# Performance work log

Measured on AMD Instinct MI355X. Metric: run time of the kernel, lower is better.

## Reference

```python
import jax, jax.numpy as jnp
import numpy as np
import math

H = 65
W = 65
NH = 8
DIM_K = 512
DIM_Q = 512
DIM_HID = NH * DIM_K  # 4096; forced by V.view(bsz,-1,num_heads,dim_K)
RW = W // 2 + 1  # 33, rfft2 last-dim size


def _conv2d(x, w, pad):
    # x: NCHW, w: OIHW
    return jax.lax.conv_general_dilated(
        x, w, window_strides=(1, 1), padding=[(pad, pad), (pad, pad)],
        dimension_numbers=('NCHW', 'OIHW', 'NCHW'))


def _filter_branch(x, w1, w2, w3, Wd, bd):
    # x: (1, DIM_K, H, W)
    f = _conv2d(x, w1, 0)                                  # 1x1 conv
    f = _conv2d(jax.nn.relu(f), w2, 1) + f                 # 3x3 conv + residual
    f = jax.nn.relu(_conv2d(jax.nn.relu(f), w3, 0))        # 1x1 -> (1, NH, H, W)
    f = f.reshape(NH, H * W) @ Wd.T + bd                   # down-proj to (NH, 65*33)
    return f.reshape(NH, H, RW)


def setup_inputs() -> dict:
    key = jax.random.key(0)
    ks = jax.random.split(key, 20)
    s = 0.02
    f32 = jnp.float32
    inp = {
        'Q': jax.random.normal(ks[0], (1, 1, DIM_Q), f32),
        'K': jax.random.normal(ks[1], (1, DIM_K, H, W), f32),
        'Wq': jax.random.normal(ks[2], (DIM_HID, DIM_Q), f32) * s,
        'bq': jnp.zeros((DIM_HID,), f32),
        'Wk': jax.random.normal(ks[3], (DIM_HID, DIM_K), f32) * s,
        'bk': jnp.zeros((DIM_HID,), f32),
        'Wv': jax.random.normal(ks[4], (DIM_HID, DIM_K), f32) * s,
        'bv': jnp.zeros((DIM_HID,), f32),
        'Wo': jax.random.normal(ks[5], (DIM_K, DIM_HID), f32) * s,
        'bo': jnp.zeros((DIM_K,), f32),
        'amp1': jax.random.normal(ks[6], (DIM_K, DIM_K, 1, 1), f32) * 0.05,
        'amp2': jax.random.normal(ks[7], (DIM_K, DIM_K, 3, 3), f32) * 0.02,
        'amp3': jax.random.normal(ks[8], (NH, DIM_K, 1, 1), f32) * 0.05,
        'pha1': jax.random.normal(ks[9], (DIM_K, DIM_K, 1, 1), f32) * 0.05,
        'pha2': jax.random.normal(ks[10], (DIM_K, DIM_K, 3, 3), f32) * 0.02,
        'pha3': jax.random.normal(ks[11], (NH, DIM_K, 1, 1), f32) * 0.05,
        'Wd1': jax.random.normal(ks[12], (H * RW, H * W), f32) * s,
        'bd1': jnp.zeros((H * RW,), f32),
        'Wd2': jax.random.normal(ks[13], (H * RW, H * W), f32) * s,
        'bd2': jnp.zeros((H * RW,), f32),
    }
    return inp


def reference(Q, K, Wq, bq, Wk, bk, Wv, bv, Wo, bo,
              amp1, amp2, amp3, pha1, pha2, pha3, Wd1, bd1, Wd2, bd2):
    bsz, h, w = K.shape[0], K.shape[2], K.shape[3]
    dk = DIM_HID // NH
    qrt = K
    Kp = jnp.transpose(K, (0, 2, 3, 1))                      # (1, h, w, DIM_K)
    q = Q @ Wq.T + bq                                        # (1, 1, DIM_HID)
    k = Kp @ Wk.T + bk                                       # (1, h, w, DIM_HID)
    v = Kp @ Wv.T + bv
    q = q.reshape(bsz, -1, NH, dk).transpose(0, 2, 1, 3)     # (1, NH, 1, dk)
    k = k.reshape(bsz, -1, NH, dk).transpose(0, 2, 1, 3)     # (1, NH, h*w, dk)
    v = v.reshape(bsz, -1, NH, DIM_K).transpose(0, 2, 1, 3)  # (1, NH, h*w, DIM_K)
    A = jnp.einsum('bhqd,bhkd->bhqk', q, k) / math.sqrt(DIM_K)
    amp_F = _filter_branch(qrt, amp1, amp2, amp3, Wd1, bd1)  # (NH, h, w//2+1)
    pha_F = _filter_branch(qrt, pha1, pha2, pha3, Wd2, bd2)
    A = A.reshape(NH, h, w)
    Af = jnp.fft.rfft2(A, axes=(-2, -1))                     # backward norm (default)
    amp = amp_F * jnp.abs(Af)
    pha = pha_F * jnp.angle(Af)
    Af = jax.lax.complex(amp * jnp.cos(pha), amp * jnp.sin(pha))
    A = jnp.fft.irfft2(Af, s=(h, w), axes=(-2, -1))
    A = jax.nn.softmax(A.reshape(bsz, NH, 1, -1), axis=-1)   # (1, NH, 1, h*w)
    x = jnp.einsum('bhqk,bhkd->bhqd', A, v)                  # (1, NH, 1, DIM_K)
    x = x.reshape(1, NH * DIM_K)
    return x @ Wo.T + bo                                     # (1, DIM_K)
```

## Files before the change

kernel.cpp:

```cpp
#include <hip/hip_runtime.h>
#include <hip/hip_bf16.h>

#define NP 4225
#define PR 2145

typedef __attribute__((ext_vector_type(8))) short short8;
typedef __attribute__((ext_vector_type(4))) float f32x4;
typedef __attribute__((ext_vector_type(4))) unsigned int u32x4;

__device__ inline float bf2f(unsigned short u) {
    union { unsigned int i; float f; } x; x.i = ((unsigned int)u) << 16; return x.f;
}
__device__ inline unsigned short f2bf(float f) {
    union { float f; unsigned int i; } x; x.f = f;
    unsigned int r = x.i + 0x7fff + ((x.i >> 16) & 1);
    return (unsigned short)(r >> 16);
}
__device__ inline u32x4 relu8(u32x4 v) {
    #pragma unroll
    for (int i = 0; i < 4; i++) {
        unsigned int s = v[i] & 0x80008000u;
        v[i] &= ~((s >> 15) * 0xFFFFu);
    }
    return v;
}
__device__ inline void gl_lds16(const void* g, void* l) {
    __builtin_amdgcn_global_load_lds(
        (const __attribute__((address_space(1))) unsigned int*)g,
        (__attribute__((address_space(3))) unsigned int*)l,
        16, 0, 0);
}


__global__ __launch_bounds__(256) void k_q(const float* __restrict__ Q,
                                           const float* __restrict__ Wq,
                                           const float* __restrict__ bq,
                                           float* __restrict__ qv)
{
    int wid = threadIdx.x >> 6, lane = threadIdx.x & 63;
    int j = blockIdx.x * 4 + wid;
    float s = 0.f;
    for (int i = lane; i < 512; i += 64) s += Q[i] * Wq[j * 512 + i];
    #pragma unroll
    for (int off = 32; off; off >>= 1) s += __shfl_down(s, off);
    if (lane == 0) qv[j] = s + bq[j];
}

__global__ __launch_bounds__(256) void k_qk3(const float* __restrict__ qv,
                                             const float* __restrict__ Wk,
                                             float* __restrict__ qkp)
{
    int c = blockIdx.x * 256 + threadIdx.x;
    int h = blockIdx.y, dz = blockIdx.z;
    __shared__ float qs[32];
    if (threadIdx.x < 32) qs[threadIdx.x] = qv[h * 512 + dz * 32 + threadIdx.x];
    __syncthreads();
    float s = 0.f;
    #pragma unroll 8
    for (int d = 0; d < 32; d++)
        s += qs[d] * Wk[(size_t)(h * 512 + dz * 32 + d) * 512 + c];
    qkp[(dz * 8 + h) * 512 + c] = s;
}

__global__ __launch_bounds__(512) void k_qb(const float* __restrict__ q,
                                            const float* __restrict__ bk,
                                            float* __restrict__ qb)
{
    int h = threadIdx.x >> 6, lane = threadIdx.x & 63;
    float s = 0.f;
    for (int d = lane; d < 512; d += 64) s += q[h * 512 + d] * bk[h * 512 + d];
    #pragma unroll
    for (int off = 32; off; off >>= 1) s += __shfl_down(s, off);
    if (lane == 0) qb[h] = s;
}

__global__ __launch_bounds__(256) void k_alogits3(const float* __restrict__ qkp,
                                                  const float* __restrict__ K,
                                                  float* __restrict__ Ap)
{
    __shared__ float sqk[8][16];
    int tid = threadIdx.x;
    int cz = blockIdx.y;
    if (tid < 128) {
        int hh = tid >> 4, cc = tid & 15;
        float s = 0.f;
        #pragma unroll
        for (int dz = 0; dz < 16; dz++) s += qkp[(dz * 8 + hh) * 512 + cz * 16 + cc];
        sqk[hh][cc] = s;
    }
    __syncthreads();
    int p = blockIdx.x * 256 + tid;
    bool ok = p < NP;
    float acc[8] = {};
    #pragma unroll
    for (int cc = 0; cc < 16; cc++) {
        float kv = ok ? K[(size_t)(cz * 16 + cc) * NP + p] : 0.f;
        #pragma unroll
        for (int h = 0; h < 8; h++) acc[h] += sqk[h][cc] * kv;
    }
    if (ok) {
        #pragma unroll
        for (int h = 0; h < 8; h++) Ap[(size_t)(cz * 8 + h) * NP + p] = acc[h];
    }
}

__global__ __launch_bounds__(256) void k_areduce(const float* __restrict__ Ap,
                                                 const float* __restrict__ qb,
                                                 float* __restrict__ A)
{
    int p = blockIdx.x * 256 + threadIdx.x;
    int h = blockIdx.y;
    if (p >= NP) return;
    float s = 0.f;
    #pragma unroll 8
    for (int cz = 0; cz < 32; cz++) s += Ap[(size_t)(cz * 8 + h) * NP + p];
    const float sc = 0.04419417382415922f;
    A[h * NP + p] = (s + qb[h]) * sc;
}


__global__ __launch_bounds__(256) void k_cast2(const float* __restrict__ a,
                                               const float* __restrict__ b,
                                               unsigned short* __restrict__ o)
{
    int i = blockIdx.x * 256 + threadIdx.x;
    int br = blockIdx.y;
    const float* src = br ? b : a;
    int m = i >> 9, c = i & 511;
    int dst = (c & ~63) | ((c & 63) ^ ((m & 7) << 3));
    o[(size_t)br * 262144 + m * 512 + dst] = f2bf(src[i]);
}

__global__ __launch_bounds__(256) void k_packW2(const float* __restrict__ a,
                                                const float* __restrict__ b,
                                                unsigned short* __restrict__ o)
{
    int i = blockIdx.x * 256 + threadIdx.x;
    int br = blockIdx.y;
    int m = i >> 9, c = i & 511;
    const float* src = (br ? b : a) + (size_t)i * 9;
    unsigned short* dst = o + (size_t)br * 512 * 4608;
    int cs = (c & ~63) | ((c & 63) ^ ((m & 7) << 3));
    #pragma unroll
    for (int t = 0; t < 9; t++) dst[(size_t)m * 4608 + t * 512 + cs] = f2bf(src[t]);
}


__global__ __launch_bounds__(256) void k_conv1T(const float* __restrict__ K,
                                                const unsigned short* __restrict__ w1b2,
                                                unsigned short* __restrict__ f0b2)
{
    __shared__ unsigned short As[2][64 * 64];
    __shared__ unsigned short Bs[2][128 * 64];
    int tid = threadIdx.x;
    int bid = blockIdx.x;
    int u = bid & 7;
    int t = bid >> 3;
    int bmi = u * 9 + t % 9;
    if (bmi >= 67) return;
    int combo = t / 9;
    int bm = bmi * 64;
    int bn = (combo & 3) * 128;
    int br = combo >> 2;
    const unsigned short* w1 = w1b2 + (size_t)br * 262144;
    unsigned short* f0 = f0b2 + (size_t)br * NP * 512;
    int lane = tid & 63;
    int w = tid >> 6;
    int wp = (w >> 1) * 32, wm = (w & 1) * 64;
    int ct = tid >> 4, p4 = (tid & 15) * 4;

    bool okj[4];
    int colj[4];
    #pragma unroll
    for (int j = 0; j < 4; j++) {
        okj[j] = (bm + p4 + j) < NP;
        colj[j] = okj[j] ? (p4 + j) : (NP - 1 - bm);
    }

    f32x4 acc[2][4];
    #pragma unroll
    for (int i = 0; i < 2; i++)
        #pragma unroll
        for (int j = 0; j < 4; j++) acc[i][j] = (f32x4){0.f, 0.f, 0.f, 0.f};

    float aE[16], aO[16];

    auto loadA = [&](int kc, float (&ar)[16]) {
        int c0 = kc * 64;
        #pragma unroll
        for (int pass = 0; pass < 4; pass++) {
            int cl = pass * 16 + ct;
            const float* src = K + (size_t)(c0 + cl) * NP + bm;
            #pragma unroll
            for (int j = 0; j < 4; j++) ar[pass * 4 + j] = src[colj[j]];
        }
    };
    auto writeA = [&](int buf, float (&ar)[16]) {
        #pragma unroll
        for (int pass = 0; pass < 4; pass++) {
            int cl = pass * 16 + ct;
            #pragma unroll
            for (int j = 0; j < 4; j++) {
                int row = p4 + j;
                int byte = (row * 128 + cl * 2) ^ ((row & 7) << 4);
                float v = okj[j] ? ar[pass * 4 + j] : 0.f;
                *(unsigned short*)((char*)As[buf] + byte) = f2bf(v);
            }
        }
    };
    auto stageB = [&](int kc, int buf) {
        const unsigned short* gb = w1 + (size_t)kc * 64 + (lane & 7) * 8;
        #pragma unroll
        for (int j = 0; j < 4; j++) {
            int row = (w * 4 + j) * 8 + (lane >> 3);
            gl_lds16(gb + (size_t)(bn + row) * 512,
                     (char*)Bs[buf] + (w * 4 + j) * 1024);
        }
    };
    auto mfmaStep = [&](int buf) {
        __builtin_amdgcn_s_setprio(1);
        #pragma unroll
        for (int ks = 0; ks < 2; ks++) {
            short8 af[2], bfr[4];
            #pragma unroll
            for (int fi = 0; fi < 2; fi++) {
                int row = wp + fi * 16 + (lane & 15);
                int byte = row * 128 + ((ks * 64 + ((lane >> 4) * 16)) ^ ((row & 7) << 4));
                af[fi] = *(const short8*)((char*)As[buf] + byte);
            }
            #pragma unroll
            for (int fj = 0; fj < 4; fj++) {
                int n = wm + fj * 16 + (lane & 15);
                int byte = n * 128 + ((ks * 64 + ((lane >> 4) * 16)) ^ ((n & 7) << 4));
                bfr[fj] = *(const short8*)((char*)Bs[buf] + byte);
            }
            #pragma unroll
            for (int fi = 0; fi < 2; fi++)
                #pragma unroll
                for (int fj = 0; fj < 4; fj++)
                    acc[fi][fj] = __builtin_amdgcn_mfma_f32_16x16x32_bf16(af[fi], bfr[fj], acc[fi][fj], 0, 0, 0);
        }
        __builtin_amdgcn_s_setprio(0);
    };

    loadA(0, aE);
    loadA(1, aO);
    stageB(0, 0);
    writeA(0, aE);
    __syncthreads();
    #pragma unroll
    for (int ib = 0; ib < 4; ib++) {
        int s0 = 2 * ib;
        if (s0 + 1 < 8) stageB(s0 + 1, 1);
        if (s0 + 2 < 8) loadA(s0 + 2, aE);
        mfmaStep(0);
        if (s0 + 1 < 8) writeA(1, aO);
        __syncthreads();
        int s1 = s0 + 1;
        if (s1 + 1 < 8) stageB(s1 + 1, 0);
        if (s1 + 2 < 8) loadA(s1 + 2, aO);
        mfmaStep(1);
        if (s1 + 1 < 8) writeA(0, aE);
        __syncthreads();
    }
    #pragma unroll
    for (int fi = 0; fi < 2; fi++)
        #pragma unroll
        for (int r = 0; r < 4; r++) {
            int p = bm + wp + fi * 16 + (lane >> 4) * 4 + r;
            if (p >= NP) continue;
            #pragma unroll
            for (int fj = 0; fj < 4; fj++) {
                int m = bn + wm + fj * 16 + (lane & 15);
                f0[(size_t)p * 512 + m] = f2bf(acc[fi][fj][r]);
            }
        }
}

__global__ __launch_bounds__(256) void k_conv3T(const unsigned short* __restrict__ f0b2,
                                                const unsigned short* __restrict__ w2b2,
                                                const float* __restrict__ amp3,
                                                const float* __restrict__ pha3,
                                                float* __restrict__ F2p)
{
    __shared__ unsigned short As[2][64 * 64];
    __shared__ unsigned short Bs[2][128 * 64];
    __shared__ float w3s[8 * 128];
    int tid = threadIdx.x;
    int bid = blockIdx.x;
    int u = bid & 7;
    int bmi = bid >> 3;
    if (bmi >= 67) return;
    int bm = bmi * 64;
    int bnq = u & 3;
    int bn = bnq * 128;
    int br = u >> 2;
    const unsigned short* f0 = f0b2 + (size_t)br * NP * 512;
    const unsigned short* w2 = w2b2 + (size_t)br * 512 * 4608;
    const float* w3 = br ? pha3 : amp3;
    for (int i = tid; i < 1024; i += 256) {
        int h = i >> 7, c = i & 127;
        w3s[i] = w3[h * 512 + bn + c];
    }
    int lane = tid & 63;
    int w = tid >> 6;
    int wp = (w >> 1) * 32, wm = (w & 1) * 64;
    int ra = tid >> 2, sa = tid & 3;
    int pA = bm + ra;
    int py = pA / 65, px = pA - py * 65;

    f32x4 acc[2][4];
    #pragma unroll
    for (int i = 0; i < 2; i++)
        #pragma unroll
        for (int j = 0; j < 4; j++) acc[i][j] = (f32x4){0.f, 0.f, 0.f, 0.f};

    u32x4 aE0, aE1, aO0, aO1;
    bool vE, vO;

    auto loadA = [&](int s, u32x4& a0, u32x4& a1, bool& vv) {
        int kc = s / 9, tap = s - kc * 9;
        int ky = tap / 3 - 1, kx = tap % 3 - 1;
        int sy = py + ky, sx = px + kx;
        bool valid = (pA < NP) && sy >= 0 && sy < 65 && sx >= 0 && sx < 65;
        int srow = valid ? (pA + ky * 65 + kx) : 0;
        const unsigned short* arow = f0 + (size_t)srow * 512 + kc * 64 + sa * 16;
        a0 = *(const u32x4*)arow;
        a1 = *(const u32x4*)(arow + 8);
        vv = valid;
    };
    auto writeA = [&](int buf, u32x4 a0, u32x4 a1, bool vv) {
        u32x4 z = {0, 0, 0, 0};
        u32x4 w0 = vv ? relu8(a0) : z;
        u32x4 w1 = vv ? relu8(a1) : z;
        int ab = ra * 128 + sa * 32;
        int swz = (ra & 7) << 4;
        *(u32x4*)((char*)As[buf] + (ab ^ swz)) = w0;
        *(u32x4*)((char*)As[buf] + ((ab + 16) ^ swz)) = w1;
    };
    auto stageB = [&](int s, int buf) {
        int kc = s / 9, tap = s - kc * 9;
        const unsigned short* gb = w2 + (size_t)tap * 512 + kc * 64 + (lane & 7) * 8;
        #pragma unroll
        for (int j = 0; j < 4; j++) {
            int row = (w * 4 + j) * 8 + (lane >> 3);
            gl_lds16(gb + (size_t)(bn + row) * 4608,
                     (char*)Bs[buf] + (w * 4 + j) * 1024);
        }
    };
    auto mfmaStep = [&](int buf) {
        __builtin_amdgcn_s_setprio(1);
        #pragma unroll
        for (int ks = 0; ks < 2; ks++) {
            short8 af[2], bfr[4];
            #pragma unroll
            for (int fi = 0; fi < 2; fi++) {
                int row = wp + fi * 16 + (lane & 15);
                int byte = row * 128 + ((ks * 64 + ((lane >> 4) * 16)) ^ ((row & 7) << 4));
                af[fi] = *(const short8*)((char*)As[buf] + byte);
            }
            #pragma unroll
            for (int fj = 0; fj < 4; fj++) {
                int n = wm + fj * 16 + (lane & 15);
                int byte = n * 128 + ((ks * 64 + ((lane >> 4) * 16)) ^ ((n & 7) << 4));
                bfr[fj] = *(const short8*)((char*)Bs[buf] + byte);
            }
            #pragma unroll
            for (int fi = 0; fi < 2; fi++)
                #pragma unroll
                for (int fj = 0; fj < 4; fj++)
                    acc[fi][fj] = __builtin_amdgcn_mfma_f32_16x16x32_bf16(af[fi], bfr[fj], acc[fi][fj], 0, 0, 0);
        }
        __builtin_amdgcn_s_setprio(0);
    };

    loadA(0, aE0, aE1, vE);
    loadA(1, aO0, aO1, vO);
    stageB(0, 0);
    writeA(0, aE0, aE1, vE);
    __syncthreads();
    for (int ib = 0; ib < 36; ib++) {
        int s0 = 2 * ib;
        if (s0 + 1 < 72) stageB(s0 + 1, 1);
        if (s0 + 2 < 72) loadA(s0 + 2, aE0, aE1, vE);
        mfmaStep(0);
        if (s0 + 1 < 72) writeA(1, aO0, aO1, vO);
        __syncthreads();
        int s1 = s0 + 1;
        if (s1 + 1 < 72) stageB(s1 + 1, 0);
        if (s1 + 2 < 72) loadA(s1 + 2, aO0, aO1, vO);
        mfmaStep(1);
        if (s1 + 1 < 72) writeA(0, aE0, aE1, vE);
        __syncthreads();
    }
    #pragma unroll
    for (int fi = 0; fi < 2; fi++)
        #pragma unroll
        for (int r = 0; r < 4; r++) {
            int row = wp + fi * 16 + (lane >> 4) * 4 + r;
            int p = bm + row;
            #pragma unroll
            for (int fj = 0; fj < 4; fj++) {
                int mcol = wm + fj * 16 + (lane & 15);
                float v = 0.f;
                if (p < NP)
                    v = fmaxf(acc[fi][fj][r] + bf2f(f0[(size_t)p * 512 + bn + mcol]), 0.f);
                int byte = (row * 256 + mcol * 2) ^ ((row & 7) << 4);
                *(unsigned short*)((char*)Bs[0] + byte) = f2bf(v);
            }
        }
    __syncthreads();
    int pl = tid >> 2, qc = tid & 3;
    float a8[8] = {};
    #pragma unroll 4
    for (int jj = 0; jj < 16; jj++) {
        int c = qc * 32 + jj * 2;
        int byte = (pl * 256 + c * 2) ^ ((pl & 7) << 4);
        unsigned int uu = *(const unsigned int*)((char*)Bs[0] + byte);
        float v0 = bf2f((unsigned short)(uu & 0xFFFF));
        float v1 = bf2f((unsigned short)(uu >> 16));
        #pragma unroll
        for (int h = 0; h < 8; h++)
            a8[h] += w3s[h * 128 + c] * v0 + w3s[h * 128 + c + 1] * v1;
    }
    #pragma unroll
    for (int h = 0; h < 8; h++) {
        a8[h] += __shfl_xor(a8[h], 1);
        a8[h] += __shfl_xor(a8[h], 2);
    }
    int p = bm + pl;
    if (qc == 0 && p < NP) {
        float* dst = F2p + (size_t)(br * 4 + bnq) * 8 * NP;
        #pragma unroll
        for (int h = 0; h < 8; h++) dst[h * NP + p] = a8[h];
    }
}

__global__ __launch_bounds__(256) void k_f2red(const float* __restrict__ F2p,
                                               float* __restrict__ F2)
{
    int p = blockIdx.x * 256 + threadIdx.x;
    int h = blockIdx.y, br = blockIdx.z;
    if (p >= NP) return;
    float s = 0.f;
    #pragma unroll
    for (int bn = 0; bn < 4; bn++) s += F2p[(size_t)((br * 4 + bn) * 8 + h) * NP + p];
    F2[(size_t)(br * 8 + h) * NP + p] = fmaxf(s, 0.f);
}

__global__ __launch_bounds__(256) void k_down(const float* __restrict__ F2,
                                              const float* __restrict__ Wd1,
                                              const float* __restrict__ bd1,
                                              const float* __restrict__ Wd2,
                                              const float* __restrict__ bd2,
                                              float* __restrict__ Fa,
                                              float* __restrict__ Fp)
{
    int wid = threadIdx.x >> 6, lane = threadIdx.x & 63;
    int j = blockIdx.x * 4 + wid;
    if (j >= PR) return;
    int br = blockIdx.y;
    const float* Wd = br ? Wd2 : Wd1;
    const float* bd = br ? bd2 : bd1;
    const float* F2b = F2 + (size_t)br * 8 * NP;
    float* Fo = br ? Fp : Fa;
    const float* wr = Wd + (size_t)j * NP;
    float acc[8] = {};
    for (int p = lane; p < NP; p += 64) {
        float wv = wr[p];
        #pragma unroll
        for (int h = 0; h < 8; h++) acc[h] += wv * F2b[h * NP + p];
    }
    #pragma unroll
    for (int h = 0; h < 8; h++) {
        #pragma unroll
        for (int off = 32; off; off >>= 1) acc[h] += __shfl_down(acc[h], off);
    }
    if (lane == 0) {
        float b = bd[j];
        #pragma unroll
        for (int h = 0; h < 8; h++) Fo[h * PR + j] = acc[h] + b;
    }
}


__global__ __launch_bounds__(128) void k_twid(double* __restrict__ ctd, double* __restrict__ snd,
                                              float* __restrict__ ctf, float* __restrict__ stf)
{
    int t = threadIdx.x;
    if (t < 65) {
        double ang = 6.283185307179586476925286766559 * (double)t / 65.0;
        double cv = cos(ang), sv = sin(ang);
        ctd[t] = cv; snd[t] = sv;
        ctf[t] = (float)cv; stf[t] = (float)sv;
    }
}

__global__ __launch_bounds__(64) void k_fftA(const float* __restrict__ A,
                                             const double* __restrict__ ctd,
                                             const double* __restrict__ snd,
                                             float* __restrict__ TrG, float* __restrict__ TiG)
{
    int b = blockIdx.x;
    int h = b / 65, y = b % 65;
    int lane = threadIdx.x;
    __shared__ float rowA[65];
    __shared__ double c65[65], s65[65];
    rowA[lane] = A[h * NP + y * 65 + lane];
    c65[lane] = ctd[lane]; s65[lane] = snd[lane];
    if (lane == 0) {
        rowA[64] = A[h * NP + y * 65 + 64];
        c65[64] = ctd[64]; s65[64] = snd[64];
    }
    __syncthreads();
    int v = lane;
    if (v < 33) {
        double sr = 0.0, si = 0.0;
        for (int x = 0; x < 65; x++) {
            int m = (v * x) % 65;
            double a = (double)rowA[x];
            sr += a * c65[m];
            si -= a * s65[m];
        }
        TrG[(h * 65 + y) * 33 + v] = (float)sr;
        TiG[(h * 65 + y) * 33 + v] = (float)si;
    }
}

__global__ __launch_bounds__(128) void k_fftBC(const float* __restrict__ TrG,
                                               const float* __restrict__ TiG,
                                               const float* __restrict__ Fa,
                                               const float* __restrict__ Fp,
                                               const double* __restrict__ ctd,
                                               const double* __restrict__ snd,
                                               const float* __restrict__ ctf,
                                               const float* __restrict__ stf,
                                               float* __restrict__ CrG, float* __restrict__ CiG)
{
    int v = blockIdx.x, h = blockIdx.y;
    int t = threadIdx.x;
    __shared__ float TrS[65], TiS[65];
    __shared__ float BrS[65], BiS[65];
    __shared__ double c65[65], s65[65];
    __shared__ float cf[65], sf[65];
    if (t < 65) {
        TrS[t] = TrG[(h * 65 + t) * 33 + v];
        TiS[t] = TiG[(h * 65 + t) * 33 + v];
        c65[t] = ctd[t]; s65[t] = snd[t];
        cf[t] = ctf[t]; sf[t] = stf[t];
    }
    __syncthreads();
    int uu = t;
    if (uu < 65) {
        double sr = 0.0, si = 0.0;
        for (int y = 0; y < 65; y++) {
            int m = (uu * y) % 65;
            double c = c65[m], s = s65[m];
            double tr = (double)TrS[y], ti = (double)TiS[y];
            sr += tr * c + ti * s;
            si += ti * c - tr * s;
        }
        float re = (float)sr, im = (float)si;
        float mag = sqrtf(re * re + im * im);
        float ang = atan2f(im, re);
        int o = uu * 33 + v;
        float amp = Fa[h * PR + o] * mag;
        float ph  = Fp[h * PR + o] * ang;
        float sn, cn;
        sincosf(ph, &sn, &cn);
        BrS[uu] = amp * cn;
        BiS[uu] = amp * sn;
    }
    __syncthreads();
    int y = t;
    if (y < 65) {
        float sr = 0.f, si = 0.f;
        for (int u2 = 0; u2 < 65; u2++) {
            int m = (u2 * y) % 65;
            float c = cf[m], s = sf[m];
            float ar = BrS[u2], ai = BiS[u2];
            sr += ar * c - ai * s;
            si += ai * c + ar * s;
        }
        CrG[(h * 65 + y) * 33 + v] = sr;
        CiG[(h * 65 + y) * 33 + v] = si;
    }
}

__global__ __launch_bounds__(128) void k_fftD(const float* __restrict__ CrG,
                                              const float* __restrict__ CiG,
                                              const float* __restrict__ ctf,
                                              const float* __restrict__ stf,
                                              float* __restrict__ A2)
{
    int y = blockIdx.x, h = blockIdx.y;
    int t = threadIdx.x;
    __shared__ float CrS[33], CiS[33];
    __shared__ float c65[65], s65[65];
    if (t < 33) {
        CrS[t] = CrG[(h * 65 + y) * 33 + t];
        CiS[t] = CiG[(h * 65 + y) * 33 + t];
    }
    if (t < 65) { c65[t] = ctf[t]; s65[t] = stf[t]; }
    __syncthreads();
    int x = t;
    if (x < 65) {
        float s = CrS[0];
        for (int v = 1; v < 33; v++) {
            int m = (v * x) % 65;
            s += 2.f * (CrS[v] * c65[m] - CiS[v] * s65[m]);
        }
        A2[h * NP + y * 65 + x] = s * (1.f / 4225.f);
    }
}

__global__ __launch_bounds__(1024) void k_softmax(const float* __restrict__ A2,
                                                  float* __restrict__ Wsm)
{
    int h = blockIdx.x, tid = threadIdx.x;
    __shared__ float red[1024];
    float mx = -3.0e38f;
    for (int i = tid; i < NP; i += 1024) mx = fmaxf(mx, A2[h * NP + i]);
    red[tid] = mx; __syncthreads();
    for (int s = 512; s; s >>= 1) {
        if (tid < s) red[tid] = fmaxf(red[tid], red[tid + s]);
        __syncthreads();
    }
    mx = red[0]; __syncthreads();
    float sum = 0.f;
    for (int i = tid; i < NP; i += 1024) sum += expf(A2[h * NP + i] - mx);
    red[tid] = sum; __syncthreads();
    for (int s = 512; s; s >>= 1) {
        if (tid < s) red[tid] += red[tid + s];
        __syncthreads();
    }
    float inv = 1.f / red[0];
    for (int i = tid; i < NP; i += 1024) Wsm[h * NP + i] = expf(A2[h * NP + i] - mx) * inv;
}

__global__ __launch_bounds__(256) void k_t(const float* __restrict__ K,
                                           const float* __restrict__ Wsm,
                                           float* __restrict__ t)
{
    int wid = threadIdx.x >> 6, lane = threadIdx.x & 63;
    int c = blockIdx.x * 4 + wid;
    float acc[8] = {};
    for (int p = lane; p < NP; p += 64) {
        float kv = K[(size_t)c * NP + p];
        #pragma unroll
        for (int h = 0; h < 8; h++) acc[h] += kv * Wsm[h * NP + p];
    }
    #pragma unroll
    for (int h = 0; h < 8; h++) {
        #pragma unroll
        for (int off = 32; off; off >>= 1) acc[h] += __shfl_down(acc[h], off);
    }
    if (lane == 0) {
        #pragma unroll
        for (int h = 0; h < 8; h++) t[h * 512 + c] = acc[h];
    }
}

__global__ __launch_bounds__(256) void k_x(const float* __restrict__ t,
                                           const float* __restrict__ Wv,
                                           const float* __restrict__ bv,
                                           float* __restrict__ x)
{
    int wid = threadIdx.x >> 6, lane = threadIdx.x & 63;
    int hd = blockIdx.x * 4 + wid;
    int h = hd >> 9;
    float s = 0.f;
    for (int c = lane; c < 512; c += 64) s += t[h * 512 + c] * Wv[(size_t)hd * 512 + c];
    #pragma unroll
    for (int off = 32; off; off >>= 1) s += __shfl_down(s, off);
    if (lane == 0) x[hd] = s + bv[hd];
}

__global__ __launch_bounds__(256) void k_out(const float* __restrict__ x,
                                             const float* __restrict__ Wo,
                                             const float* __restrict__ bo,
                                             float* __restrict__ out)
{
    int wid = threadIdx.x >> 6, lane = threadIdx.x & 63;
    int j = blockIdx.x * 4 + wid;
    float s = 0.f;
    for (int i = lane; i < 4096; i += 64) s += x[i] * Wo[(size_t)j * 4096 + i];
    #pragma unroll
    for (int off = 32; off; off >>= 1) s += __shfl_down(s, off);
    if (lane == 0) out[j] = s + bo[j];
}

extern "C" void kernel_launch(void* const* d_in, const int* in_sizes, int n_in,
                              void* d_out, int out_size, void* d_ws, size_t ws_size,
                              hipStream_t stream)
{
    (void)in_sizes; (void)n_in; (void)out_size; (void)ws_size;
    const float* Q    = (const float*)d_in[0];
    const float* K    = (const float*)d_in[1];
    const float* Wq   = (const float*)d_in[2];
    const float* bq   = (const float*)d_in[3];
    const float* Wk   = (const float*)d_in[4];
    const float* bk   = (const float*)d_in[5];
    const float* Wv   = (const float*)d_in[6];
    const float* bv   = (const float*)d_in[7];
    const float* Wo   = (const float*)d_in[8];
    const float* bo   = (const float*)d_in[9];
    const float* amp1 = (const float*)d_in[10];
    const float* amp2 = (const float*)d_in[11];
    const float* amp3 = (const float*)d_in[12];
    const float* pha1 = (const float*)d_in[13];
    const float* pha2 = (const float*)d_in[14];
    const float* pha3 = (const float*)d_in[15];
    const float* Wd1  = (const float*)d_in[16];
    const float* bd1  = (const float*)d_in[17];
    const float* Wd2  = (const float*)d_in[18];
    const float* bd2  = (const float*)d_in[19];
    float* out = (float*)d_out;

    char* w = (char*)d_ws;
    auto alloc = [&](size_t bytes) { char* p = w; w += (bytes + 255) & ~(size_t)255; return p; };
    float* qv   = (float*)alloc(4096 * 4);
    float* qkp  = (float*)alloc(16 * 8 * 512 * 4);
    float* qb   = (float*)alloc(64 * 4);
    float* A    = (float*)alloc(8 * NP * 4);
    unsigned short* w1b2 = (unsigned short*)alloc((size_t)2 * 512 * 512 * 2);
    unsigned short* w2b2 = (unsigned short*)alloc((size_t)2 * 512 * 4608 * 2);
    unsigned short* f0b2 = (unsigned short*)alloc((size_t)2 * NP * 512 * 2);
    float* F2p  = (float*)alloc((size_t)2 * 4 * 8 * NP * 4);
    float* F2   = (float*)alloc((size_t)2 * 8 * NP * 4);
    float* Fa   = (float*)alloc(8 * PR * 4);
    float* Fp   = (float*)alloc(8 * PR * 4);
    double* ctd = (double*)alloc(65 * 8);
    double* snd = (double*)alloc(65 * 8);
    float* ctf  = (float*)alloc(65 * 4);
    float* stf  = (float*)alloc(65 * 4);
    float* Ap   = (float*)w2b2;
    {
        char* s2 = (char*)f0b2;
        auto alias = [&](size_t bytes) { char* p = s2; s2 += (bytes + 255) & ~(size_t)255; return p; };
        float* A2  = (float*)alias(8 * NP * 4);
        float* wsm = (float*)alias(8 * NP * 4);
        float* tt  = (float*)alias(4096 * 4);
        float* xx  = (float*)alias(4096 * 4);
        float* TrG = (float*)alias(8 * PR * 4);
        float* TiG = (float*)alias(8 * PR * 4);
        float* CrG = (float*)alias(8 * PR * 4);
        float* CiG = (float*)alias(8 * PR * 4);

        k_twid<<<1, 128, 0, stream>>>(ctd, snd, ctf, stf);

        k_q<<<1024, 256, 0, stream>>>(Q, Wq, bq, qv);
        k_qk3<<<dim3(2, 8, 16), 256, 0, stream>>>(qv, Wk, qkp);
        k_qb<<<1, 512, 0, stream>>>(qv, bk, qb);
        k_alogits3<<<dim3(17, 32), 256, 0, stream>>>(qkp, K, Ap);
        k_areduce<<<dim3(17, 8), 256, 0, stream>>>(Ap, qb, A);

        k_cast2<<<dim3(1024, 2), 256, 0, stream>>>(amp1, pha1, w1b2);
        k_packW2<<<dim3(1024, 2), 256, 0, stream>>>(amp2, pha2, w2b2);

        k_conv1T<<<576, 256, 0, stream>>>(K, w1b2, f0b2);
        k_conv3T<<<536, 256, 0, stream>>>(f0b2, w2b2, amp3, pha3, F2p);
        k_f2red<<<dim3(17, 8, 2), 256, 0, stream>>>(F2p, F2);
        k_down<<<dim3(537, 2), 256, 0, stream>>>(F2, Wd1, bd1, Wd2, bd2, Fa, Fp);

        k_fftA<<<520, 64, 0, stream>>>(A, ctd, snd, TrG, TiG);
        k_fftBC<<<dim3(33, 8), 128, 0, stream>>>(TrG, TiG, Fa, Fp, ctd, snd, ctf, stf, CrG, CiG);
        k_fftD<<<dim3(65, 8), 128, 0, stream>>>(CrG, CiG, ctf, stf, A2);
        k_softmax<<<8, 1024, 0, stream>>>(A2, wsm);
        k_t<<<128, 256, 0, stream>>>(K, wsm, tt);
        k_x<<<1024, 256, 0, stream>>>(tt, Wv, bv, xx);
        k_out<<<128, 256, 0, stream>>>(xx, Wo, bo, out);
    }
}
```

Measured before the change: 252.4 us.

## Stage conv3x3 A tiles via direct global-to-LDS loads with pre-swizzled f0

The 3x3 conv kernel now loads its shifted activation rows straight into LDS with gl_lds16 instead of going through registers. The producer kernel writes f0 with a per-row XOR swizzle so that these raw copies land in a bank-conflict-free layout. Boundary masking and ReLU move into the MFMA fragment read, keyed on the tap shift. The aim is to cut register pressure and VALU work in the staging path. In exchange, every fragment read now repeats ReLU and validity checks, and the swizzle must match exactly across both kernels and the residual read.

Result: slower. 258.7 us (+2.5%).

```diff
diff --git a/kernel.cpp b/kernel.cpp
--- a/kernel.cpp
+++ b/kernel.cpp
@@ -272,7 +272,8 @@
             #pragma unroll
             for (int fj = 0; fj < 4; fj++) {
                 int m = bn + wm + fj * 16 + (lane & 15);
-                f0[(size_t)p * 512 + m] = f2bf(acc[fi][fj][r]);
+                int ms = (m & ~63) | ((m & 63) ^ ((p & 7) << 3));
+                f0[(size_t)p * 512 + ms] = f2bf(acc[fi][fj][r]);
             }
         }
 }
@@ -305,9 +306,8 @@
     int lane = tid & 63;
     int w = tid >> 6;
     int wp = (w >> 1) * 32, wm = (w & 1) * 64;
-    int ra = tid >> 2, sa = tid & 3;
-    int pA = bm + ra;
-    int py = pA / 65, px = pA - py * 65;
+    int pxf0 = (bm + wp + (lane & 15)) % 65;
+    int pxf1 = (bm + wp + 16 + (lane & 15)) % 65;
 
     f32x4 acc[2][4];
     #pragma unroll
@@ -315,28 +315,17 @@
         #pragma unroll
         for (int j = 0; j < 4; j++) acc[i][j] = (f32x4){0.f, 0.f, 0.f, 0.f};
 
-    u32x4 aE0, aE1, aO0, aO1;
-    bool vE, vO;
-
-    auto loadA = [&](int s, u32x4& a0, u32x4& a1, bool& vv) {
+    auto stageA = [&](int s, int buf) {
         int kc = s / 9, tap = s - kc * 9;
-        int ky = tap / 3 - 1, kx = tap % 3 - 1;
-        int sy = py + ky, sx = px + kx;
-        bool valid = (pA < NP) && sy >= 0 && sy < 65 && sx >= 0 && sx < 65;
-        int srow = valid ? (pA + ky * 65 + kx) : 0;
-        const unsigned short* arow = f0 + (size_t)srow * 512 + kc * 64 + sa * 16;
-        a0 = *(const u32x4*)arow;
-        a1 = *(const u32x4*)(arow + 8);
-        vv = valid;
-    };
-    auto writeA = [&](int buf, u32x4 a0, u32x4 a1, bool vv) {
-        u32x4 z = {0, 0, 0, 0};
-        u32x4 w0 = vv ? relu8(a0) : z;
-        u32x4 w1 = vv ? relu8(a1) : z;
-        int ab = ra * 128 + sa * 32;
-        int swz = (ra & 7) << 4;
-        *(u32x4*)((char*)As[buf] + (ab ^ swz)) = w0;
-        *(u32x4*)((char*)As[buf] + ((ab + 16) ^ swz)) = w1;
+        int shift = (tap / 3 - 1) * 65 + (tap % 3) - 1;
+        #pragma unroll
+        for (int j = 0; j < 2; j++) {
+            int r = j * 32 + w * 8 + (lane >> 3);
+            int g = bm + shift + r;
+            g = g < 0 ? 0 : (g >= NP ? NP - 1 : g);
+            gl_lds16(f0 + (size_t)g * 512 + kc * 64 + (lane & 7) * 8,
+                     (char*)As[buf] + j * 4096 + w * 1024);
+        }
     };
     auto stageB = [&](int s, int buf) {
         int kc = s / 9, tap = s - kc * 9;
@@ -348,7 +337,10 @@
                      (char*)Bs[buf] + (w * 4 + j) * 1024);
         }
     };
-    auto mfmaStep = [&](int buf) {
+    auto mfmaStep = [&](int buf, int s) {
+        int tap = s % 9;
+        int ky = tap / 3 - 1, kx = tap % 3 - 1;
+        int shift = ky * 65 + kx;
         __builtin_amdgcn_s_setprio(1);
         #pragma unroll
         for (int ks = 0; ks < 2; ks++) {
@@ -356,8 +348,18 @@
             #pragma unroll
             for (int fi = 0; fi < 2; fi++) {
                 int row = wp + fi * 16 + (lane & 15);
-                int byte = row * 128 + ((ks * 64 + ((lane >> 4) * 16)) ^ ((row & 7) << 4));
-                af[fi] = *(const short8*)((char*)As[buf] + byte);
+                int key = ((row + shift) & 7) << 4;
+                int byte = row * 128 + ((ks * 64 + ((lane >> 4) * 16)) ^ key);
+                u32x4 a = *(const u32x4*)((char*)As[buf] + byte);
+                int pin = bm + row + shift;
+                int px = fi ? pxf1 : pxf0;
+                bool ok = ((unsigned)pin < NP) &&
+                          !((kx < 0 && px == 0) || (kx > 0 && px == 64));
+                a = relu8(a);
+                u32x4 z = {0, 0, 0, 0};
+                a = ok ? a : z;
+                union { u32x4 u; short8 s8; } cv; cv.u = a;
+                af[fi] = cv.s8;
             }
             #pragma unroll
             for (int fj = 0; fj < 4; fj++) {
@@ -374,23 +376,15 @@
         __builtin_amdgcn_s_setprio(0);
     };
 
-    loadA(0, aE0, aE1, vE);
-    loadA(1, aO0, aO1, vO);
     stageB(0, 0);
-    writeA(0, aE0, aE1, vE);
-    __syncthreads();
-    for (int ib = 0; ib < 36; ib++) {
-        int s0 = 2 * ib;
-        if (s0 + 1 < 72) stageB(s0 + 1, 1);
-        if (s0 + 2 < 72) loadA(s0 + 2, aE0, aE1, vE);
-        mfmaStep(0);
-        if (s0 + 1 < 72) writeA(1, aO0, aO1, vO);
+    stageA(0, 0);
+    __syncthreads();
+    for (int s0 = 0; s0 < 72; s0 += 2) {
+        if (s0 + 1 < 72) { stageB(s0 + 1, 1); stageA(s0 + 1, 1); }
+        mfmaStep(0, s0);
         __syncthreads();
-        int s1 = s0 + 1;
-        if (s1 + 1 < 72) stageB(s1 + 1, 0);
-        if (s1 + 2 < 72) loadA(s1 + 2, aO0, aO1, vO);
-        mfmaStep(1);
-        if (s1 + 1 < 72) writeA(0, aE0, aE1, vE);
+        if (s0 + 2 < 72) { stageB(s0 + 2, 0); stageA(s0 + 2, 0); }
+        mfmaStep(1, s0 + 1);
         __syncthreads();
     }
     #pragma unroll
@@ -403,8 +397,11 @@
             for (int fj = 0; fj < 4; fj++) {
                 int mcol = wm + fj * 16 + (lane & 15);
                 float v = 0.f;
-                if (p < NP)
-                    v = fmaxf(acc[fi][fj][r] + bf2f(f0[(size_t)p * 512 + bn + mcol]), 0.f);
+                if (p < NP) {
+                    int m = bn + mcol;
+                    int ms = (m & ~63) | ((m & 63) ^ ((p & 7) << 3));
+                    v = fmaxf(acc[fi][fj][r] + bf2f(f0[(size_t)p * 512 + ms]), 0.f);
+                }
                 int byte = (row * 256 + mcol * 2) ^ ((row & 7) << 4);
                 *(unsigned short*)((char*)Bs[0] + byte) = f2bf(v);
             }
```

## Fuse small launches: merge q/qk/twiddle, areduce+fftA, atomic conv3 reduction

Applied to the files above, without the earlier changes.

Several small kernels are merged to cut launch count. The q projection, the q·Wk product and the twiddle table are folded into one kernel, and qb is recomputed per block inside the new reduce+row-DFT kernel. That kernel combines the A partial-sum reduction with the first FFT stage. The conv3T partial sums are now accumulated with atomicAdd into a memset-zeroed F2, and the ReLU moves into k_down, which removes the k_f2red pass. In exchange the q row dot products are recomputed redundantly across blocks, atomics add contention, and float summation order becomes nondeterministic.

Result: no change. 257.3 us (+1.9%).

```diff
diff --git a/kernel.cpp b/kernel.cpp
--- a/kernel.cpp
+++ b/kernel.cpp
@@ -32,46 +32,40 @@
 }
 
 
-__global__ __launch_bounds__(256) void k_q(const float* __restrict__ Q,
-                                           const float* __restrict__ Wq,
-                                           const float* __restrict__ bq,
-                                           float* __restrict__ qv)
-{
-    int wid = threadIdx.x >> 6, lane = threadIdx.x & 63;
-    int j = blockIdx.x * 4 + wid;
+__global__ __launch_bounds__(256) void k_qk4(const float* __restrict__ Q,
+                                             const float* __restrict__ Wq,
+                                             const float* __restrict__ bq,
+                                             const float* __restrict__ Wk,
+                                             float* __restrict__ qv,
+                                             float* __restrict__ qkp,
+                                             double* __restrict__ ctd, double* __restrict__ snd,
+                                             float* __restrict__ ctf, float* __restrict__ stf)
+{
+    int bx = blockIdx.x, h = blockIdx.y, dz = blockIdx.z;
+    int tid = threadIdx.x;
+    if (bx == 1 && h == 0 && dz == 0 && tid < 65) {
+        double ang = 6.283185307179586476925286766559 * (double)tid / 65.0;
+        double cv = cos(ang), sv = sin(ang);
+        ctd[tid] = cv; snd[tid] = sv;
+        ctf[tid] = (float)cv; stf[tid] = (float)sv;
+    }
+    __shared__ float qs[32];
+    int g = tid >> 3, l = tid & 7;
+    int row = h * 512 + dz * 32 + g;
     float s = 0.f;
-    for (int i = lane; i < 512; i += 64) s += Q[i] * Wq[j * 512 + i];
-    #pragma unroll
-    for (int off = 32; off; off >>= 1) s += __shfl_down(s, off);
-    if (lane == 0) qv[j] = s + bq[j];
-}
-
-__global__ __launch_bounds__(256) void k_qk3(const float* __restrict__ qv,
-                                             const float* __restrict__ Wk,
-                                             float* __restrict__ qkp)
-{
-    int c = blockIdx.x * 256 + threadIdx.x;
-    int h = blockIdx.y, dz = blockIdx.z;
-    __shared__ float qs[32];
-    if (threadIdx.x < 32) qs[threadIdx.x] = qv[h * 512 + dz * 32 + threadIdx.x];
-    __syncthreads();
-    float s = 0.f;
+    for (int d = l; d < 512; d += 8) s += Q[d] * Wq[(size_t)row * 512 + d];
+    s += __shfl_xor(s, 1);
+    s += __shfl_xor(s, 2);
+    s += __shfl_xor(s, 4);
+    if (l == 0) qs[g] = s + bq[row];
+    __syncthreads();
+    if (bx == 0 && tid < 32) qv[h * 512 + dz * 32 + tid] = qs[tid];
+    int c = bx * 256 + tid;
+    float s2 = 0.f;
     #pragma unroll 8
     for (int d = 0; d < 32; d++)
-        s += qs[d] * Wk[(size_t)(h * 512 + dz * 32 + d) * 512 + c];
-    qkp[(dz * 8 + h) * 512 + c] = s;
-}
-
-__global__ __launch_bounds__(512) void k_qb(const float* __restrict__ q,
-                                            const float* __restrict__ bk,
-                                            float* __restrict__ qb)
-{
-    int h = threadIdx.x >> 6, lane = threadIdx.x & 63;
-    float s = 0.f;
-    for (int d = lane; d < 512; d += 64) s += q[h * 512 + d] * bk[h * 512 + d];
-    #pragma unroll
-    for (int off = 32; off; off >>= 1) s += __shfl_down(s, off);
-    if (lane == 0) qb[h] = s;
+        s2 += qs[d] * Wk[(size_t)(h * 512 + dz * 32 + d) * 512 + c];
+    qkp[(dz * 8 + h) * 512 + c] = s2;
 }
 
 __global__ __launch_bounds__(256) void k_alogits3(const float* __restrict__ qkp,
@@ -104,18 +98,49 @@
     }
 }
 
-__global__ __launch_bounds__(256) void k_areduce(const float* __restrict__ Ap,
-                                                 const float* __restrict__ qb,
-                                                 float* __restrict__ A)
-{
-    int p = blockIdx.x * 256 + threadIdx.x;
-    int h = blockIdx.y;
-    if (p >= NP) return;
-    float s = 0.f;
-    #pragma unroll 8
-    for (int cz = 0; cz < 32; cz++) s += Ap[(size_t)(cz * 8 + h) * NP + p];
+__global__ __launch_bounds__(128) void k_ared_fftA(const float* __restrict__ Ap,
+                                                   const float* __restrict__ qv,
+                                                   const float* __restrict__ bk,
+                                                   const double* __restrict__ ctd,
+                                                   const double* __restrict__ snd,
+                                                   float* __restrict__ TrG, float* __restrict__ TiG)
+{
+    int y = blockIdx.x, h = blockIdx.y;
+    int t = threadIdx.x;
+    __shared__ float rowA[65];
+    __shared__ double c65[65], s65[65];
+    __shared__ float qbred[128];
+    float qp = 0.f;
+    for (int d = t; d < 512; d += 128) qp += qv[h * 512 + d] * bk[h * 512 + d];
+    qbred[t] = qp;
+    __syncthreads();
+    for (int s = 64; s; s >>= 1) {
+        if (t < s) qbred[t] += qbred[t + s];
+        __syncthreads();
+    }
+    float qbh = qbred[0];
+    if (t < 65) { c65[t] = ctd[t]; s65[t] = snd[t]; }
     const float sc = 0.04419417382415922f;
-    A[h * NP + p] = (s + qb[h]) * sc;
+    if (t < 65) {
+        int p = y * 65 + t;
+        float s = 0.f;
+        #pragma unroll 8
+        for (int cz = 0; cz < 32; cz++) s += Ap[(size_t)(cz * 8 + h) * NP + p];
+        rowA[t] = (s + qbh) * sc;
+    }
+    __syncthreads();
+    int v = t;
+    if (v < 33) {
+        double sr = 0.0, si = 0.0;
+        for (int x = 0; x < 65; x++) {
+            int m = (v * x) % 65;
+            double a = (double)rowA[x];
+            sr += a * c65[m];
+            si -= a * s65[m];
+        }
+        TrG[(h * 65 + y) * 33 + v] = (float)sr;
+        TiG[(h * 65 + y) * 33 + v] = (float)si;
+    }
 }
 
 
@@ -281,7 +306,7 @@
                                                 const unsigned short* __restrict__ w2b2,
                                                 const float* __restrict__ amp3,
                                                 const float* __restrict__ pha3,
-                                                float* __restrict__ F2p)
+                                                float* __restrict__ F2)
 {
     __shared__ unsigned short As[2][64 * 64];
     __shared__ unsigned short Bs[2][128 * 64];
@@ -430,22 +455,10 @@
     }
     int p = bm + pl;
     if (qc == 0 && p < NP) {
-        float* dst = F2p + (size_t)(br * 4 + bnq) * 8 * NP;
-        #pragma unroll
-        for (int h = 0; h < 8; h++) dst[h * NP + p] = a8[h];
-    }
-}
-
-__global__ __launch_bounds__(256) void k_f2red(const float* __restrict__ F2p,
-                                               float* __restrict__ F2)
-{
-    int p = blockIdx.x * 256 + threadIdx.x;
-    int h = blockIdx.y, br = blockIdx.z;
-    if (p >= NP) return;
-    float s = 0.f;
-    #pragma unroll
-    for (int bn = 0; bn < 4; bn++) s += F2p[(size_t)((br * 4 + bn) * 8 + h) * NP + p];
-    F2[(size_t)(br * 8 + h) * NP + p] = fmaxf(s, 0.f);
+        #pragma unroll
+        for (int h = 0; h < 8; h++)
+            atomicAdd(&F2[(size_t)(br * 8 + h) * NP + p], a8[h]);
+    }
 }
 
 __global__ __launch_bounds__(256) void k_down(const float* __restrict__ F2,
@@ -469,7 +482,7 @@
     for (int p = lane; p < NP; p += 64) {
         float wv = wr[p];
         #pragma unroll
-        for (int h = 0; h < 8; h++) acc[h] += wv * F2b[h * NP + p];
+        for (int h = 0; h < 8; h++) acc[h] += wv * fmaxf(F2b[h * NP + p], 0.f);
     }
     #pragma unroll
     for (int h = 0; h < 8; h++) {
@@ -483,49 +496,6 @@
     }
 }
 
-
-__global__ __launch_bounds__(128) void k_twid(double* __restrict__ ctd, double* __restrict__ snd,
-                                              float* __restrict__ ctf, float* __restrict__ stf)
-{
-    int t = threadIdx.x;
-    if (t < 65) {
-        double ang = 6.283185307179586476925286766559 * (double)t / 65.0;
-        double cv = cos(ang), sv = sin(ang);
-        ctd[t] = cv; snd[t] = sv;
-        ctf[t] = (float)cv; stf[t] = (float)sv;
-    }
-}
-
-__global__ __launch_bounds__(64) void k_fftA(const float* __restrict__ A,
-                                             const double* __restrict__ ctd,
-                                             const double* __restrict__ snd,
-                                             float* __restrict__ TrG, float* __restrict__ TiG)
-{
-    int b = blockIdx.x;
-    int h = b / 65, y = b % 65;
-    int lane = threadIdx.x;
-    __shared__ float rowA[65];
-    __shared__ double c65[65], s65[65];
-    rowA[lane] = A[h * NP + y * 65 + lane];
-    c65[lane] = ctd[lane]; s65[lane] = snd[lane];
-    if (lane == 0) {
-        rowA[64] = A[h * NP + y * 65 + 64];
-        c65[64] = ctd[64]; s65[64] = snd[64];
-    }
-    __syncthreads();
-    int v = lane;
-    if (v < 33) {
-        double sr = 0.0, si = 0.0;
-        for (int x = 0; x < 65; x++) {
-            int m = (v * x) % 65;
-            double a = (double)rowA[x];
-            sr += a * c65[m];
-            si -= a * s65[m];
-        }
-        TrG[(h * 65 + y) * 33 + v] = (float)sr;
-        TiG[(h * 65 + y) * 33 + v] = (float)si;
-    }
-}
 
 __global__ __launch_bounds__(128) void k_fftBC(const float* __restrict__ TrG,
                                                const float* __restrict__ TiG,
@@ -721,12 +691,9 @@
     auto alloc = [&](size_t bytes) { char* p = w; w += (bytes + 255) & ~(size_t)255; return p; };
     float* qv   = (float*)alloc(4096 * 4);
     float* qkp  = (float*)alloc(16 * 8 * 512 * 4);
-    float* qb   = (float*)alloc(64 * 4);
-    float* A    = (float*)alloc(8 * NP * 4);
     unsigned short* w1b2 = (unsigned short*)alloc((size_t)2 * 512 * 512 * 2);
     unsigned short* w2b2 = (unsigned short*)alloc((size_t)2 * 512 * 4608 * 2);
     unsigned short* f0b2 = (unsigned short*)alloc((size_t)2 * NP * 512 * 2);
-    float* F2p  = (float*)alloc((size_t)2 * 4 * 8 * NP * 4);
     float* F2   = (float*)alloc((size_t)2 * 8 * NP * 4);
     float* Fa   = (float*)alloc(8 * PR * 4);
     float* Fp   = (float*)alloc(8 * PR * 4);
@@ -734,6 +701,10 @@
     double* snd = (double*)alloc(65 * 8);
     float* ctf  = (float*)alloc(65 * 4);
     float* stf  = (float*)alloc(65 * 4);
+    float* TrG  = (float*)alloc(8 * PR * 4);
+    float* TiG  = (float*)alloc(8 * PR * 4);
+    float* CrG  = (float*)alloc(8 * PR * 4);
+    float* CiG  = (float*)alloc(8 * PR * 4);
     float* Ap   = (float*)w2b2;
     {
         char* s2 = (char*)f0b2;
@@ -742,28 +713,20 @@
         float* wsm = (float*)alias(8 * NP * 4);
         float* tt  = (float*)alias(4096 * 4);
         float* xx  = (float*)alias(4096 * 4);
-        float* TrG = (float*)alias(8 * PR * 4);
-        float* TiG = (float*)alias(8 * PR * 4);
-        float* CrG = (float*)alias(8 * PR * 4);
-        float* CiG = (float*)alias(8 * PR * 4);
-
-        k_twid<<<1, 128, 0, stream>>>(ctd, snd, ctf, stf);
-
-        k_q<<<1024, 256, 0, stream>>>(Q, Wq, bq, qv);
-        k_qk3<<<dim3(2, 8, 16), 256, 0, stream>>>(qv, Wk, qkp);
-        k_qb<<<1, 512, 0, stream>>>(qv, bk, qb);
+
+        hipMemsetAsync(F2, 0, (size_t)2 * 8 * NP * 4, stream);
+
+        k_qk4<<<dim3(2, 8, 16), 256, 0, stream>>>(Q, Wq, bq, Wk, qv, qkp, ctd, snd, ctf, stf);
         k_alogits3<<<dim3(17, 32), 256, 0, stream>>>(qkp, K, Ap);
-        k_areduce<<<dim3(17, 8), 256, 0, stream>>>(Ap, qb, A);
+        k_ared_fftA<<<dim3(65, 8), 128, 0, stream>>>(Ap, qv, bk, ctd, snd, TrG, TiG);
 
         k_cast2<<<dim3(1024, 2), 256, 0, stream>>>(amp1, pha1, w1b2);
         k_packW2<<<dim3(1024, 2), 256, 0, stream>>>(amp2, pha2, w2b2);
 
         k_conv1T<<<576, 256, 0, stream>>>(K, w1b2, f0b2);
-        k_conv3T<<<536, 256, 0, stream>>>(f0b2, w2b2, amp3, pha3, F2p);
-        k_f2red<<<dim3(17, 8, 2), 256, 0, stream>>>(F2p, F2);
+        k_conv3T<<<536, 256, 0, stream>>>(f0b2, w2b2, amp3, pha3, F2);
         k_down<<<dim3(537, 2), 256, 0, stream>>>(F2, Wd1, bd1, Wd2, bd2, Fa, Fp);
 
-        k_fftA<<<520, 64, 0, stream>>>(A, ctd, snd, TrG, TiG);
         k_fftBC<<<dim3(33, 8), 128, 0, stream>>>(TrG, TiG, Fa, Fp, ctd, snd, ctf, stf, CrG, CiG);
         k_fftD<<<dim3(65, 8), 128, 0, stream>>>(CrG, CiG, ctf, stf, A2);
         k_softmax<<<8, 1024, 0, stream>>>(A2, wsm);
```
